# Kernel optimization log

Measured on AMD Instinct MI355X. Metric: run time of the kernel, lower is better.

The kernel has to match this reference:

```python
import jax, jax.numpy as jnp
import numpy as np

B, P_LEN, Q_LEN, D, H = 16, 128, 256, 128, 128


def setup_inputs() -> dict:
    key = jax.random.key(0)
    ks = jax.random.split(key, 16)
    s = 0.05
    inp = {
        "p": jax.random.normal(ks[0], (B, P_LEN, D), dtype=jnp.float32),
        "q": jax.random.normal(ks[1], (B, Q_LEN, D), dtype=jnp.float32),
        # attention linears: W_s, W_t (D->H), W_r (H->H), W_e (H->1)
        "Ws_w": jax.random.normal(ks[2], (H, D), dtype=jnp.float32) * s,
        "Ws_b": jnp.zeros((H,), dtype=jnp.float32),
        "Wt_w": jax.random.normal(ks[3], (H, D), dtype=jnp.float32) * s,
        "Wt_b": jnp.zeros((H,), dtype=jnp.float32),
        "Wr_w": jax.random.normal(ks[4], (H, H), dtype=jnp.float32) * s,
        "Wr_b": jnp.zeros((H,), dtype=jnp.float32),
        "We_w": jax.random.normal(ks[5], (H,), dtype=jnp.float32) * s,
        "We_b": jax.random.normal(ks[6], (), dtype=jnp.float32) * s,
        # input gate linear: (D+H)->(D+H)
        "Wg_w": jax.random.normal(ks[7], (D + H, D + H), dtype=jnp.float32) * s,
        "Wg_b": jnp.zeros((D + H,), dtype=jnp.float32),
        # LSTMCell: gates ordered i,f,g,o as in torch
        "Wih": jax.random.normal(ks[8], (4 * H, D + H), dtype=jnp.float32) * s,
        "Whh": jax.random.normal(ks[9], (4 * H, H), dtype=jnp.float32) * s,
        "bih": jnp.zeros((4 * H,), dtype=jnp.float32),
        "bhh": jnp.zeros((4 * H,), dtype=jnp.float32),
        # entity_embedding=None -> these int ids are unused pass-throughs
        "p_seq": jax.random.randint(ks[10], (B, P_LEN), 0, 10000, dtype=jnp.int64) if jax.config.jax_enable_x64 else jax.random.randint(ks[10], (B, P_LEN), 0, 10000, dtype=jnp.int32),
        "q_seq": jax.random.randint(ks[11], (B, Q_LEN), 0, 10000, dtype=jnp.int32),
    }
    return inp


def _mlstm(p, q, Ws_w, Ws_b, Wt_w, Wt_b, Wr_w, Wr_b, We_w, We_b,
           Wg_w, Wg_b, Wih, Whh, bih, bhh):
    # precompute W_s(q): [B, Q, H] (loop-invariant)
    W_hs = jnp.einsum('bqd,hd->bqh', q, Ws_w) + Ws_b
    h0 = jnp.zeros((p.shape[0], H), dtype=p.dtype)
    c0 = jnp.zeros_like(h0)

    def step(carry, p_pos):  # p_pos: [B, D]
        h, c = carry
        # TriMatchAttention (entity_embedding=None)
        w_ht = p_pos @ Wt_w.T + Wt_b            # [B, H]
        w_hm = h @ Wr_w.T + Wr_b                # [B, H]
        s = jnp.tanh(W_hs + (w_ht + w_hm)[:, None, :])   # [B, Q, H]
        score = jnp.einsum('bqh,h->bq', s, We_w) + We_b  # [B, Q]
        a = jax.nn.softmax(score, axis=1)                # [B, Q]
        alpha = jnp.einsum('bq,bqh->bh', a, W_hs)        # [B, H]
        x = jnp.concatenate([alpha, p_pos], axis=1)      # [B, H+D]
        # gate (IsGate=True)
        g_t = jax.nn.sigmoid(x @ Wg_w.T + Wg_b)
        x = g_t * x
        # LSTMCell
        gates = x @ Wih.T + bih + h @ Whh.T + bhh        # [B, 4H]
        i, f, g, o = jnp.split(gates, 4, axis=1)
        c_new = jax.nn.sigmoid(f) * c + jax.nn.sigmoid(i) * jnp.tanh(g)
        h_new = jax.nn.sigmoid(o) * jnp.tanh(c_new)
        return (h_new, c_new), h_new

    _, hs = jax.lax.scan(step, (h0, c0), jnp.swapaxes(p, 0, 1))  # hs: [P, B, H]
    return jnp.swapaxes(hs, 0, 1)  # [B, P, H] == stacked h_states[1:]


def reference(p, q, Ws_w, Ws_b, Wt_w, Wt_b, Wr_w, Wr_b, We_w, We_b,
              Wg_w, Wg_b, Wih, Whh, bih, bhh, p_seq, q_seq):
    # p_seq/q_seq unused: entity_embedding=None in TriMatchAttention
    return _mlstm(p, q, Ws_w, Ws_b, Wt_w, Wt_b, Wr_w, Wr_b, We_w, We_b,
                  Wg_w, Wg_b, Wih, Whh, bih, bhh)
```

## Files before the change

kernel.cpp:

```cpp
#include <hip/hip_runtime.h>
#include <hip/hip_fp16.h>
#include <cstdint>


__device__ __forceinline__ float bf2f(uint16_t u) {
  uint32_t x = ((uint32_t)u) << 16; float f; __builtin_memcpy(&f, &x, 4); return f;
}
__device__ __forceinline__ float load_in(const void* p, size_t i, int f32) {
  return f32 ? ((const float*)p)[i] : bf2f(((const uint16_t*)p)[i]);
}
__device__ __forceinline__ float frcp(float x) { return __builtin_amdgcn_rcpf(x); }
__device__ __forceinline__ float tanh_fast(float x) {
  float E = __expf(2.0f * x);
  return 1.0f - 2.0f * frcp(E + 1.0f);
}
__device__ __forceinline__ float sigm(float x) { return frcp(1.0f + __expf(-x)); }
__device__ __forceinline__ float2 h2f(uint32_t u) {
  __half2 h; __builtin_memcpy(&h, &u, 4); return __half22float2(h);
}
__device__ __forceinline__ uint32_t f2h(float a, float b) {
  __half2 h = __floats2half2_rn(a, b);
  uint32_t u; __builtin_memcpy(&u, &h, 4); return u;
}

typedef _Float16 h2v __attribute__((ext_vector_type(2)));
__device__ __forceinline__ float dot2(uint32_t w, uint32_t x, float acc) {
#if defined(__has_builtin)
#if __has_builtin(__builtin_amdgcn_fdot2)
  h2v a, b; __builtin_memcpy(&a, &w, 4); __builtin_memcpy(&b, &x, 4);
  return __builtin_amdgcn_fdot2(a, b, acc, false);
#else
  float2 af = h2f(w), bf = h2f(x);
  return fmaf(af.x, bf.x, fmaf(af.y, bf.y, acc));
#endif
#else
  float2 af = h2f(w), bf = h2f(x);
  return fmaf(af.x, bf.x, fmaf(af.y, bf.y, acc));
#endif
}

__global__ void detect_kernel(const uint16_t* __restrict__ q16,
                              uint32_t* __restrict__ flag) {
  __shared__ int cnt;
  if (threadIdx.x == 0) cnt = 0;
  __syncthreads();
  int bad = 0;
  for (int i = threadIdx.x; i < 4096; i += 256) {
    int e = (q16[i] >> 7) & 0xFF;
    if (e > 0x8A) bad++;
  }
  atomicAdd(&cnt, bad);
  __syncthreads();
  if (threadIdx.x == 0) *flag = (cnt > 16) ? 1u : 0u;
}

__global__ void pack2(const void* __restrict__ p,
                      const void* __restrict__ Wr,  const void* __restrict__ Wrb_,
                      const void* __restrict__ Wew_, const void* __restrict__ Web_,
                      const void* __restrict__ Wg,
                      const void* __restrict__ Wih, const void* __restrict__ Whh,
                      const void* __restrict__ bih, const void* __restrict__ bhh,
                      float* __restrict__ pf,
                      uint32_t* __restrict__ WrP, float* __restrict__ wrb,
                      float* __restrict__ wew, float* __restrict__ web,
                      uint32_t* __restrict__ WgP, uint32_t* __restrict__ WTP,
                      float* __restrict__ bbv,
                      const uint32_t* __restrict__ flag) {
  const int f32 = (int)*flag;
  long idx = (long)blockIdx.x * blockDim.x + threadIdx.x;
  if (idx < 262144) { pf[idx] = load_in(p, idx, f32); return; }
  idx -= 262144;
  if (idx < 8192) {
    int c = (int)(idx >> 2), w = (int)(idx & 3);
    int i = c >> 10, t = c & 1023;
    int jA = t >> 3, kgA = t & 7;
    int k = kgA * 16 + i * 8 + w * 2;
    WrP[idx] = f2h(load_in(Wr, (size_t)jA * 128 + k, f32),
                   load_in(Wr, (size_t)jA * 128 + k + 1, f32));
    return; }
  idx -= 8192;
  if (idx < 128) { wrb[idx] = load_in(Wrb_, idx, f32); return; }
  idx -= 128;
  if (idx < 128) { wew[idx] = load_in(Wew_, idx, f32); return; }
  idx -= 128;
  if (idx < 1) { web[0] = load_in(Web_, 0, f32); return; }
  idx -= 1;
  if (idx < 16384) {
    int c = (int)(idx >> 2), w = (int)(idx & 3);
    int i = c >> 10, t = c & 1023;
    int iE = t >> 2, kgE = t & 3;
    int k = kgE * 32 + i * 8 + w * 2;
    WgP[idx] = f2h(load_in(Wg, (size_t)iE * 256 + k, f32),
                   load_in(Wg, (size_t)iE * 256 + k + 1, f32));
    return; }
  idx -= 16384;
  if (idx < 98304) {
    int c = (int)(idx >> 2), w = (int)(idx & 3);
    int i = c >> 10, t = c & 1023;
    int iF = t >> 1, kgF = t & 1;
    int k = kgF * 192 + i * 8 + w * 2;
    float v0 = (k < 256) ? load_in(Wih, (size_t)iF * 256 + k, f32)
                         : load_in(Whh, (size_t)iF * 128 + (k - 256), f32);
    float v1 = (k + 1 < 256) ? load_in(Wih, (size_t)iF * 256 + k + 1, f32)
                             : load_in(Whh, (size_t)iF * 128 + (k + 1 - 256), f32);
    WTP[idx] = f2h(v0, v1);
    return; }
  idx -= 98304;
  if (idx < 512) { bbv[idx] = load_in(bih, idx, f32) + load_in(bhh, idx, f32); }
}

__global__ __launch_bounds__(256) void gemm3(
    const void* __restrict__ q, const void* __restrict__ p,
    const void* __restrict__ Wsw, const void* __restrict__ Wsb,
    const void* __restrict__ Wtw, const void* __restrict__ Wtb,
    const void* __restrict__ Wgw, const void* __restrict__ Wgb,
    float* __restrict__ whs, float* __restrict__ wht, float* __restrict__ Gp,
    const uint32_t* __restrict__ flag) {
  __shared__ float A_l[16][128];
  __shared__ float W_l[64][129];
  const int f32 = (int)*flag;
  const int t = threadIdx.x;
  const void* A; const void* W; const void* bias; float* out;
  int lda = 128, ldw, w_off, C, r0;
  int blk = blockIdx.x;
  if (blk < 256)      { A = q; W = Wsw; bias = Wsb; out = whs; ldw = 128; w_off = 0;   C = 128; r0 = blk * 16; }
  else if (blk < 384) { A = p; W = Wtw; bias = Wtb; out = wht; ldw = 128; w_off = 0;   C = 128; r0 = (blk - 256) * 16; }
  else                { A = p; W = Wgw; bias = Wgb; out = Gp;  ldw = 256; w_off = 128; C = 256; r0 = (blk - 384) * 16; }
  for (int idx = t; idx < 16 * 128; idx += 256) {
    int rr = idx >> 7, kk = idx & 127;
    A_l[rr][kk] = load_in(A, (size_t)(r0 + rr) * lda + kk, f32);
  }
  const int c_l = t & 63, rg = t >> 6;
  for (int c0 = 0; c0 < C; c0 += 64) {
    __syncthreads();
    for (int idx = t; idx < 64 * 128; idx += 256) {
      int cc = idx >> 7, kk = idx & 127;
      W_l[cc][kk] = load_in(W, (size_t)w_off + (size_t)(c0 + cc) * ldw + kk, f32);
    }
    __syncthreads();
    float acc[4] = {0.f, 0.f, 0.f, 0.f};
    for (int k = 0; k < 128; k++) {
      float w = W_l[c_l][k];
#pragma unroll
      for (int x = 0; x < 4; x++) acc[x] = fmaf(A_l[rg * 4 + x][k], w, acc[x]);
    }
    float bv = load_in(bias, c0 + c_l, f32);
#pragma unroll
    for (int x = 0; x < 4; x++)
      out[(size_t)(r0 + rg * 4 + x) * C + c0 + c_l] = acc[x] + bv;
  }
}

__global__ void tapack(const float* __restrict__ whs, uint32_t* __restrict__ TAp) {
  int o = blockIdx.x * 256 + threadIdx.x;
  int b = o >> 14, r = o & 16383;
  int c = r >> 2, w = r & 3;
  int i = c >> 10, t = c & 1023;
  int qB = t >> 2, hgB = t & 3;
  int h = hgB * 32 + i * 8 + w * 2;
  const float* base = whs + ((size_t)b * 256 + qB) * 128 + h;
  TAp[o] = f2h(tanhf(base[0]), tanhf(base[1]));
}

#define TUIDX(j) ((((j) >> 5) * 36) + ((j) & 31))
#define SCIDX(q) ((((q) >> 5) * 36) + ((q) & 31))
#define AIDX(h)  ((((h) >> 5) * 36) + ((h) & 31))
#define HIDX(k)  ((((k) >> 4) * 20) + ((k) & 15))

__global__ __launch_bounds__(1024) void mlstm_seq11(
    const float* __restrict__ pf,
    const float* __restrict__ whs,
    const float* __restrict__ wht_g,
    const float* __restrict__ Gp_g,
    const uint32_t* __restrict__ WrP,
    const float* __restrict__ wrb,
    const float* __restrict__ wew,
    const float* __restrict__ web,
    const uint32_t* __restrict__ WgP,
    const uint32_t* __restrict__ WTP,
    const uint32_t* __restrict__ TAp,
    const float* __restrict__ bbv,
    float* __restrict__ out) {
  const int b = blockIdx.x, t = threadIdx.x;

  __shared__ __align__(16) float whs_l[256 * 132];
  __shared__ __align__(16) uint32_t xh_h2[192];
  __shared__ __align__(16) float tu_s[144];
  __shared__ __align__(16) float wew_s[144];
  __shared__ __align__(16) float sc_s[288];
  __shared__ __align__(16) float e_s[256];
  __shared__ __align__(16) float alpha_s[144];
  __shared__ __align__(16) float h_s[160];
  __shared__ __align__(16) float gates_s[512];
  __shared__ float inv_s;

  const float* whs_b = whs + (size_t)b * 32768;

  const int jA = t >> 3, kgA = t & 7;
  const int qB = t >> 2, hgB = t & 3;
  const int hD = t >> 3, qgD = t & 7;
  const int iE = t >> 2, kgE = t & 3;
  const int iF = t >> 1, kgF = t & 1;

  for (int i4 = t; i4 < 8192; i4 += 1024)
    *(float4*)(whs_l + (i4 >> 5) * 132 + ((i4 & 31) << 2)) =
        *(const float4*)(whs_b + ((size_t)i4 << 2));
  if (t < 128) wew_s[TUIDX(t)] = wew[t];
  if (t < 160) h_s[t] = 0.f;
  if (t < 64) xh_h2[128 + t] = 0u;

  const float wrb_r = wrb[jA];
  const float web_r = web[0];
  const float bbF_r = bbv[iF];
  float c_r = 0.f;

  const uint4* wrp4 = (const uint4*)WrP;
  const uint4* wgp4 = (const uint4*)WgP;
  const uint4* wtp4 = (const uint4*)WTP;
  const uint4* tap4 = (const uint4*)TAp + (size_t)b * 4096;

  float wht_c = (kgA == 0) ? wht_g[((size_t)b * 128 + 0) * 128 + jA] : 0.f;
  float gp_c  = (kgE == 0) ? Gp_g[((size_t)b * 128 + 0) * 256 + iE] : 0.f;
  float pf_c  = (kgE == 0 && iE >= 128) ? pf[((size_t)b * 128 + 0) * 128 + (iE - 128)] : 0.f;

  __syncthreads();

  for (int st = 0; st < 128; st++) {
    const int st1 = (st < 127) ? st + 1 : 127;
    float wht_n = (kgA == 0) ? wht_g[((size_t)b * 128 + st1) * 128 + jA] : 0.f;
    float gp_n  = (kgE == 0) ? Gp_g[((size_t)b * 128 + st1) * 256 + iE] : 0.f;
    float pf_n  = (kgE == 0 && iE >= 128) ? pf[((size_t)b * 128 + st1) * 128 + (iE - 128)] : 0.f;

    {
      float acc = 0.f;
#pragma unroll
      for (int i = 0; i < 2; i++) {
        uint4 wv = wrp4[i * 1024 + t];
        const float* hp = h_s + kgA * 20 + i * 8;
        float4 hA = *(const float4*)(hp);
        float4 hB = *(const float4*)(hp + 4);
        float2 w0 = h2f(wv.x), w1 = h2f(wv.y), w2 = h2f(wv.z), w3 = h2f(wv.w);
        acc = fmaf(hA.x, w0.x, acc); acc = fmaf(hA.y, w0.y, acc);
        acc = fmaf(hA.z, w1.x, acc); acc = fmaf(hA.w, w1.y, acc);
        acc = fmaf(hB.x, w2.x, acc); acc = fmaf(hB.y, w2.y, acc);
        acc = fmaf(hB.z, w3.x, acc); acc = fmaf(hB.w, w3.y, acc);
      }
      acc += __shfl_xor(acc, 1);
      acc += __shfl_xor(acc, 2);
      acc += __shfl_xor(acc, 4);
      if (kgA == 0) tu_s[TUIDX(jA)] = tanh_fast(acc + wrb_r + wht_c);
    }
    __syncthreads();

    {
      float acc = 0.f;
#pragma unroll
      for (int i = 0; i < 4; i++) {
        uint4 av = tap4[i * 1024 + t];
        const float* up = tu_s + hgB * 36 + i * 8;
        const float* wp = wew_s + hgB * 36 + i * 8;
        float4 uA = *(const float4*)(up);
        float4 uB = *(const float4*)(up + 4);
        float4 wA = *(const float4*)(wp);
        float4 wB = *(const float4*)(wp + 4);
        float2 a0 = h2f(av.x), a1 = h2f(av.y), a2 = h2f(av.z), a3 = h2f(av.w);
        acc = fmaf((a0.x + uA.x) * frcp(fmaxf(fmaf(a0.x, uA.x, 1.f), 1e-6f)), wA.x, acc);
        acc = fmaf((a0.y + uA.y) * frcp(fmaxf(fmaf(a0.y, uA.y, 1.f), 1e-6f)), wA.y, acc);
        acc = fmaf((a1.x + uA.z) * frcp(fmaxf(fmaf(a1.x, uA.z, 1.f), 1e-6f)), wA.z, acc);
        acc = fmaf((a1.y + uA.w) * frcp(fmaxf(fmaf(a1.y, uA.w, 1.f), 1e-6f)), wA.w, acc);
        acc = fmaf((a2.x + uB.x) * frcp(fmaxf(fmaf(a2.x, uB.x, 1.f), 1e-6f)), wB.x, acc);
        acc = fmaf((a2.y + uB.y) * frcp(fmaxf(fmaf(a2.y, uB.y, 1.f), 1e-6f)), wB.y, acc);
        acc = fmaf((a3.x + uB.z) * frcp(fmaxf(fmaf(a3.x, uB.z, 1.f), 1e-6f)), wB.z, acc);
        acc = fmaf((a3.y + uB.w) * frcp(fmaxf(fmaf(a3.y, uB.w, 1.f), 1e-6f)), wB.w, acc);
      }
      acc += __shfl_xor(acc, 1);
      acc += __shfl_xor(acc, 2);
      if (hgB == 0) sc_s[SCIDX(qB)] = acc + web_r;
    }
    __syncthreads();

    if (t < 64) {
      float s0 = sc_s[SCIDX(t)],       s1 = sc_s[SCIDX(t + 64)];
      float s2 = sc_s[SCIDX(t + 128)], s3 = sc_s[SCIDX(t + 192)];
      float mx = fmaxf(fmaxf(s0, s1), fmaxf(s2, s3));
#pragma unroll
      for (int d = 1; d < 64; d <<= 1) mx = fmaxf(mx, __shfl_xor(mx, d));
      float e0 = __expf(s0 - mx), e1 = __expf(s1 - mx),
            e2 = __expf(s2 - mx), e3 = __expf(s3 - mx);
      float sum = e0 + e1 + e2 + e3;
#pragma unroll
      for (int d = 1; d < 64; d <<= 1) sum += __shfl_xor(sum, d);
      e_s[t] = e0; e_s[t + 64] = e1; e_s[t + 128] = e2; e_s[t + 192] = e3;
      if (t == 0) inv_s = frcp(sum);
    }
    __syncthreads();

    {
      const float* whs_p = whs_l + qgD * 132 + hD;
      float acc = 0.f;
#pragma unroll 8
      for (int r = 0; r < 32; r++)
        acc = fmaf(e_s[qgD + 8 * r], whs_p[r * 1056], acc);
      acc += __shfl_xor(acc, 1);
      acc += __shfl_xor(acc, 2);
      acc += __shfl_xor(acc, 4);
      if (qgD == 0) alpha_s[AIDX(hD)] = acc * inv_s;
    }
    __syncthreads();

    {
      float acc = 0.f;
#pragma unroll
      for (int i = 0; i < 4; i++) {
        uint4 wv = wgp4[i * 1024 + t];
        const float* ap = alpha_s + kgE * 36 + i * 8;
        float4 aA = *(const float4*)(ap);
        float4 aB = *(const float4*)(ap + 4);
        float2 w0 = h2f(wv.x), w1 = h2f(wv.y), w2 = h2f(wv.z), w3 = h2f(wv.w);
        acc = fmaf(aA.x, w0.x, acc); acc = fmaf(aA.y, w0.y, acc);
        acc = fmaf(aA.z, w1.x, acc); acc = fmaf(aA.w, w1.y, acc);
        acc = fmaf(aB.x, w2.x, acc); acc = fmaf(aB.y, w2.y, acc);
        acc = fmaf(aB.z, w3.x, acc); acc = fmaf(aB.w, w3.y, acc);
      }
      acc += __shfl_xor(acc, 1);
      acc += __shfl_xor(acc, 2);
      float v = 0.f;
      if (kgE == 0) {
        float sg = sigm(gp_c + acc);
        float xv = (iE < 128) ? alpha_s[AIDX(iE)] : pf_c;
        v = sg * xv;
      }
      float vp = __shfl_xor(v, 4);
      if (kgE == 0 && (iE & 1) == 0) xh_h2[iE >> 1] = f2h(v, vp);
    }
    __syncthreads();

    {
      const uint4* xv4 = (const uint4*)xh_h2;
      float acc = 0.f;
#pragma unroll 8
      for (int i = 0; i < 24; i++) {
        uint4 wv = wtp4[i * 1024 + t];
        uint4 xv = xv4[kgF * 24 + i];
        acc = dot2(wv.x, xv.x, acc); acc = dot2(wv.y, xv.y, acc);
        acc = dot2(wv.z, xv.z, acc); acc = dot2(wv.w, xv.w, acc);
      }
      acc += __shfl_xor(acc, 1);
      if (kgF == 0) gates_s[iF] = acc + bbF_r;
    }
    __syncthreads();

    if (t < 128) {
      float iv = sigm(gates_s[t]);
      float fv = sigm(gates_s[128 + t]);
      float gv = tanh_fast(gates_s[256 + t]);
      float ov = sigm(gates_s[384 + t]);
      float cn = fmaf(fv, c_r, iv * gv);
      float hn = ov * tanh_fast(cn);
      c_r = cn;
      h_s[HIDX(t)] = hn;
      float hp = __shfl_xor(hn, 1);
      if ((t & 1) == 0) xh_h2[128 + (t >> 1)] = f2h(hn, hp);
      out[((size_t)b * 128 + st) * 128 + t] = hn;
    }
    __syncthreads();

    wht_c = wht_n; gp_c = gp_n; pf_c = pf_n;
  }
}

extern "C" void kernel_launch(void* const* d_in, const int* in_sizes, int n_in,
                              void* d_out, int out_size, void* d_ws, size_t ws_size,
                              hipStream_t stream) {
  static const int SZ_DICT[18] = {262144, 524288, 16384, 128, 16384, 128,
                                  16384, 128, 128, 1, 65536, 256,
                                  131072, 65536, 512, 512, 2048, 4096};
  static const int ALPHA2DICT[18] = {9, 8, 11, 10, 13, 12, 7, 6, 3, 2, 5, 4,
                                     15, 14, 0, 16, 1, 17};
  const void* in[18];
  for (int i = 0; i < 18; i++) in[i] = (i < n_in) ? d_in[i] : nullptr;

  bool dict_ok = true;
  int lim = (n_in < 16) ? n_in : 16;
  for (int i = 0; i < lim; i++) if (in_sizes[i] != SZ_DICT[i]) dict_ok = false;
  if (!dict_ok) {
    bool alpha_ok = true;
    for (int s = 0; s < n_in && s < 18; s++)
      if (in_sizes[s] != SZ_DICT[ALPHA2DICT[s]]) alpha_ok = false;
    if (alpha_ok)
      for (int s = 0; s < n_in && s < 18; s++) in[ALPHA2DICT[s]] = d_in[s];
  }

  const void* p   = in[0];  const void* q   = in[1];
  const void* Wsw = in[2];  const void* Wsb = in[3];
  const void* Wtw = in[4];  const void* Wtb = in[5];
  const void* Wrw = in[6];  const void* Wrb = in[7];
  const void* Wew = in[8];  const void* Web = in[9];
  const void* Wgw = in[10]; const void* Wgb = in[11];
  const void* Wih = in[12]; const void* Whh = in[13];
  const void* bih = in[14]; const void* bhh = in[15];

  float* ws = (float*)d_ws;
  float* whs  = ws;
  float* pff  = whs + 524288;
  float* wht  = pff + 262144;
  float* Gp   = wht + 262144;
  uint32_t* WrP = (uint32_t*)(Gp + 524288);
  uint32_t* WgP = WrP + 8192;
  uint32_t* WTP = WgP + 16384;
  uint32_t* TAp = WTP + 98304;
  float* bbv  = (float*)(TAp + 262144);
  float* wrb  = bbv + 512;
  float* wew  = wrb + 128;
  float* web  = wew + 128;
  uint32_t* flag = (uint32_t*)(web + 4);

  hipLaunchKernelGGL(detect_kernel, dim3(1), dim3(256), 0, stream,
                     (const uint16_t*)q, flag);
  hipLaunchKernelGGL(pack2, dim3(1508), dim3(256), 0, stream,
                     p, Wrw, Wrb, Wew, Web, Wgw, Wih, Whh, bih, bhh,
                     pff, WrP, wrb, wew, web, WgP, WTP, bbv, flag);
  hipLaunchKernelGGL(gemm3, dim3(512), dim3(256), 0, stream,
                     q, p, Wsw, Wsb, Wtw, Wtb, Wgw, Wgb, whs, wht, Gp, flag);
  hipLaunchKernelGGL(tapack, dim3(1024), dim3(256), 0, stream, whs, TAp);
  hipLaunchKernelGGL(mlstm_seq11, dim3(16), dim3(1024), 0, stream,
                     pff, whs, wht, Gp, WrP, wrb, wew, web, WgP, WTP, TAp, bbv,
                     (float*)d_out);
}
```

Before: 1.410 ms.

## Split LSTM gate matvec across four cooperative blocks per batch with global h exchange

The recurrent kernel now runs 64 blocks (4 per batch) instead of 16. Each block computes the LSTM gates for a 32-wide slice of the hidden state, using a re-packed weight layout and an 8-way lane reduction. The new h slices are exchanged each step through a double-buffered global array and an agent-scope atomic counter barrier. This cuts the per-block gate matvec weight traffic by four and spreads it over more CUs. In exchange it adds a cross-block spin barrier every timestep, and each block still redundantly computes the attention and gate stages.

```diff
diff --git a/kernel.cpp b/kernel.cpp
--- a/kernel.cpp
+++ b/kernel.cpp
@@ -21,6 +21,12 @@
 __device__ __forceinline__ uint32_t f2h(float a, float b) {
   __half2 h = __floats2half2_rn(a, b);
   uint32_t u; __builtin_memcpy(&u, &h, 4); return u;
+}
+__device__ __forceinline__ void st_agent(float* p, float v) {
+  __hip_atomic_store(p, v, __ATOMIC_RELAXED, __HIP_MEMORY_SCOPE_AGENT);
+}
+__device__ __forceinline__ float ld_agent(const float* p) {
+  return __hip_atomic_load(p, __ATOMIC_RELAXED, __HIP_MEMORY_SCOPE_AGENT);
 }
 
 typedef _Float16 h2v __attribute__((ext_vector_type(2)));
@@ -63,9 +69,10 @@
                       float* __restrict__ pf,
                       uint32_t* __restrict__ WrP, float* __restrict__ wrb,
                       float* __restrict__ wew, float* __restrict__ web,
-                      uint32_t* __restrict__ WgP, uint32_t* __restrict__ WTP,
+                      uint32_t* __restrict__ WgP, uint32_t* __restrict__ WTPs,
                       float* __restrict__ bbv,
-                      const uint32_t* __restrict__ flag) {
+                      const uint32_t* __restrict__ flag,
+                      float* __restrict__ hexz, uint32_t* __restrict__ ctrz) {
   const int f32 = (int)*flag;
   long idx = (long)blockIdx.x * blockDim.x + threadIdx.x;
   if (idx < 262144) { pf[idx] = load_in(p, idx, f32); return; }
@@ -96,17 +103,24 @@
   idx -= 16384;
   if (idx < 98304) {
     int c = (int)(idx >> 2), w = (int)(idx & 3);
-    int i = c >> 10, t = c & 1023;
-    int iF = t >> 1, kgF = t & 1;
-    int k = kgF * 192 + i * 8 + w * 2;
-    float v0 = (k < 256) ? load_in(Wih, (size_t)iF * 256 + k, f32)
-                         : load_in(Whh, (size_t)iF * 128 + (k - 256), f32);
-    float v1 = (k + 1 < 256) ? load_in(Wih, (size_t)iF * 256 + k + 1, f32)
-                             : load_in(Whh, (size_t)iF * 128 + (k + 1 - 256), f32);
-    WTP[idx] = f2h(v0, v1);
+    int C = c >> 10, t = c & 1023;
+    int slice = C / 6, i = C % 6;
+    int iF2 = t >> 3, kgF2 = t & 7;
+    int gate = iF2 >> 5, hl = iF2 & 31;
+    int row = gate * 128 + slice * 32 + hl;
+    int k = kgF2 * 48 + i * 8 + w * 2;
+    float v0 = (k < 256) ? load_in(Wih, (size_t)row * 256 + k, f32)
+                         : load_in(Whh, (size_t)row * 128 + (k - 256), f32);
+    float v1 = (k + 1 < 256) ? load_in(Wih, (size_t)row * 256 + k + 1, f32)
+                             : load_in(Whh, (size_t)row * 128 + (k + 1 - 256), f32);
+    WTPs[idx] = f2h(v0, v1);
     return; }
   idx -= 98304;
-  if (idx < 512) { bbv[idx] = load_in(bih, idx, f32) + load_in(bhh, idx, f32); }
+  if (idx < 512) { bbv[idx] = load_in(bih, idx, f32) + load_in(bhh, idx, f32); return; }
+  idx -= 512;
+  if (idx < 4096) { hexz[idx] = 0.f; return; }
+  idx -= 4096;
+  if (idx < 2048) { ctrz[idx] = 0u; }
 }
 
 __global__ __launch_bounds__(256) void gemm3(
@@ -167,7 +181,7 @@
 #define AIDX(h)  ((((h) >> 5) * 36) + ((h) & 31))
 #define HIDX(k)  ((((k) >> 4) * 20) + ((k) & 15))
 
-__global__ __launch_bounds__(1024) void mlstm_seq11(
+__global__ __launch_bounds__(1024) void mlstm_seq15(
     const float* __restrict__ pf,
     const float* __restrict__ whs,
     const float* __restrict__ wht_g,
@@ -177,11 +191,13 @@
     const float* __restrict__ wew,
     const float* __restrict__ web,
     const uint32_t* __restrict__ WgP,
-    const uint32_t* __restrict__ WTP,
+    const uint32_t* __restrict__ WTPs,
     const uint32_t* __restrict__ TAp,
     const float* __restrict__ bbv,
+    float* __restrict__ h_ex,
+    uint32_t* __restrict__ ctr,
     float* __restrict__ out) {
-  const int b = blockIdx.x, t = threadIdx.x;
+  const int b = blockIdx.x & 15, slice = blockIdx.x >> 4, t = threadIdx.x;
 
   __shared__ __align__(16) float whs_l[256 * 132];
   __shared__ __align__(16) uint32_t xh_h2[192];
@@ -191,7 +207,7 @@
   __shared__ __align__(16) float e_s[256];
   __shared__ __align__(16) float alpha_s[144];
   __shared__ __align__(16) float h_s[160];
-  __shared__ __align__(16) float gates_s[512];
+  __shared__ __align__(16) float gates_s[128];
   __shared__ float inv_s;
 
   const float* whs_b = whs + (size_t)b * 32768;
@@ -200,7 +216,7 @@
   const int qB = t >> 2, hgB = t & 3;
   const int hD = t >> 3, qgD = t & 7;
   const int iE = t >> 2, kgE = t & 3;
-  const int iF = t >> 1, kgF = t & 1;
+  const int iF2 = t >> 3, kgF2 = t & 7;
 
   for (int i4 = t; i4 < 8192; i4 += 1024)
     *(float4*)(whs_l + (i4 >> 5) * 132 + ((i4 & 31) << 2)) =
@@ -211,13 +227,14 @@
 
   const float wrb_r = wrb[jA];
   const float web_r = web[0];
-  const float bbF_r = bbv[iF];
+  const float bbF_r = bbv[(iF2 >> 5) * 128 + slice * 32 + (iF2 & 31)];
   float c_r = 0.f;
 
   const uint4* wrp4 = (const uint4*)WrP;
   const uint4* wgp4 = (const uint4*)WgP;
-  const uint4* wtp4 = (const uint4*)WTP;
+  const uint4* wts4 = (const uint4*)WTPs + (size_t)(slice * 6) * 1024;
   const uint4* tap4 = (const uint4*)TAp + (size_t)b * 4096;
+  uint32_t* ctr_b = ctr + b * 128;
 
   float wht_c = (kgA == 0) ? wht_g[((size_t)b * 128 + 0) * 128 + jA] : 0.f;
   float gp_c  = (kgE == 0) ? Gp_g[((size_t)b * 128 + 0) * 256 + iE] : 0.f;
@@ -338,33 +355,51 @@
     {
       const uint4* xv4 = (const uint4*)xh_h2;
       float acc = 0.f;
-#pragma unroll 8
-      for (int i = 0; i < 24; i++) {
-        uint4 wv = wtp4[i * 1024 + t];
-        uint4 xv = xv4[kgF * 24 + i];
+#pragma unroll
+      for (int i = 0; i < 6; i++) {
+        uint4 wv = wts4[i * 1024 + t];
+        uint4 xv = xv4[kgF2 * 6 + i];
         acc = dot2(wv.x, xv.x, acc); acc = dot2(wv.y, xv.y, acc);
         acc = dot2(wv.z, xv.z, acc); acc = dot2(wv.w, xv.w, acc);
       }
       acc += __shfl_xor(acc, 1);
-      if (kgF == 0) gates_s[iF] = acc + bbF_r;
-    }
-    __syncthreads();
-
-    if (t < 128) {
+      acc += __shfl_xor(acc, 2);
+      acc += __shfl_xor(acc, 4);
+      if (kgF2 == 0) gates_s[iF2] = acc + bbF_r;
+    }
+    __syncthreads();
+
+    if (t < 32) {
       float iv = sigm(gates_s[t]);
-      float fv = sigm(gates_s[128 + t]);
-      float gv = tanh_fast(gates_s[256 + t]);
-      float ov = sigm(gates_s[384 + t]);
+      float fv = sigm(gates_s[32 + t]);
+      float gv = tanh_fast(gates_s[64 + t]);
+      float ov = sigm(gates_s[96 + t]);
       float cn = fmaf(fv, c_r, iv * gv);
       float hn = ov * tanh_fast(cn);
       c_r = cn;
-      h_s[HIDX(t)] = hn;
-      float hp = __shfl_xor(hn, 1);
-      if ((t & 1) == 0) xh_h2[128 + (t >> 1)] = f2h(hn, hp);
-      out[((size_t)b * 128 + st) * 128 + t] = hn;
-    }
-    __syncthreads();
-
+      int h = slice * 32 + t;
+      st_agent(h_ex + ((st + 1) & 1) * 2048 + b * 128 + h, hn);
+      out[((size_t)b * 128 + st) * 128 + h] = hn;
+    }
+    __syncthreads();
+    if (t == 0)
+      __hip_atomic_fetch_add(ctr_b + st, 1u, __ATOMIC_RELEASE,
+                             __HIP_MEMORY_SCOPE_AGENT);
+    if (st < 127) {
+      if (t == 0) {
+        while (__hip_atomic_load(ctr_b + st, __ATOMIC_ACQUIRE,
+                                 __HIP_MEMORY_SCOPE_AGENT) < 4u)
+          __builtin_amdgcn_s_sleep(1);
+      }
+      __syncthreads();
+      if (t < 128) {
+        float hv = ld_agent(h_ex + ((st + 1) & 1) * 2048 + b * 128 + t);
+        h_s[HIDX(t)] = hv;
+        float hp = __shfl_xor(hv, 1);
+        if ((t & 1) == 0) xh_h2[128 + (t >> 1)] = f2h(hv, hp);
+      }
+      __syncthreads();
+    }
     wht_c = wht_n; gp_c = gp_n; pf_c = pf_n;
   }
 }
@@ -407,23 +442,39 @@
   float* Gp   = wht + 262144;
   uint32_t* WrP = (uint32_t*)(Gp + 524288);
   uint32_t* WgP = WrP + 8192;
-  uint32_t* WTP = WgP + 16384;
-  uint32_t* TAp = WTP + 98304;
+  uint32_t* WTPs = WgP + 16384;
+  uint32_t* TAp = WTPs + 98304;
   float* bbv  = (float*)(TAp + 262144);
   float* wrb  = bbv + 512;
   float* wew  = wrb + 128;
   float* web  = wew + 128;
   uint32_t* flag = (uint32_t*)(web + 4);
+  float* h_ex = (float*)(flag + 4);
+  uint32_t* ctrp = (uint32_t*)(h_ex + 4096);
 
   hipLaunchKernelGGL(detect_kernel, dim3(1), dim3(256), 0, stream,
                      (const uint16_t*)q, flag);
-  hipLaunchKernelGGL(pack2, dim3(1508), dim3(256), 0, stream,
+  hipLaunchKernelGGL(pack2, dim3(1532), dim3(256), 0, stream,
                      p, Wrw, Wrb, Wew, Web, Wgw, Wih, Whh, bih, bhh,
-                     pff, WrP, wrb, wew, web, WgP, WTP, bbv, flag);
+                     pff, WrP, wrb, wew, web, WgP, WTPs, bbv, flag,
+                     h_ex, ctrp);
   hipLaunchKernelGGL(gemm3, dim3(512), dim3(256), 0, stream,
                      q, p, Wsw, Wsb, Wtw, Wtb, Wgw, Wgb, whs, wht, Gp, flag);
   hipLaunchKernelGGL(tapack, dim3(1024), dim3(256), 0, stream, whs, TAp);
-  hipLaunchKernelGGL(mlstm_seq11, dim3(16), dim3(1024), 0, stream,
-                     pff, whs, wht, Gp, WrP, wrb, wew, web, WgP, WTP, TAp, bbv,
-                     (float*)d_out);
-}
+
+  float* outf = (float*)d_out;
+  const float* a0 = pff;  const float* a1 = whs;  const float* a2 = wht;
+  const float* a3 = Gp;
+  const uint32_t* a4 = WrP; const float* a5 = wrb; const float* a6 = wew;
+  const float* a7 = web;  const uint32_t* a8 = WgP;
+  const uint32_t* a9 = WTPs; const uint32_t* a10 = TAp;
+  const float* a11 = bbv; float* a12 = h_ex; uint32_t* a13 = ctrp;
+  float* a14 = outf;
+  void* kargs[15] = {
+    (void*)&a0, (void*)&a1, (void*)&a2, (void*)&a3, (void*)&a4,
+    (void*)&a5, (void*)&a6, (void*)&a7, (void*)&a8, (void*)&a9,
+    (void*)&a10, (void*)&a11, (void*)&a12, (void*)&a13, (void*)&a14
+  };
+  hipLaunchCooperativeKernel((const void*)mlstm_seq15, dim3(64), dim3(1024),
+                             kargs, 0, stream);
+}
```

Result: slower. 1.632 ms (+15.7%).
